# Optimization experiments

Hardware: AMD Instinct MI355X
Metric: run time of the kernel (lower is better)

The kernel has to match this reference:

```python
import jax, jax.numpy as jnp
import numpy as np

NUM_EXPERTS = 8
TOP_K = 2
RMS_EPS = 1e-6
SCALING = NUM_EXPERTS / TOP_K


def setup_inputs() -> dict:
    key = jax.random.key(0)
    ks = jax.random.split(key, 6)
    B, S, H, I, E = 4, 2048, 2048, 1024, NUM_EXPERTS
    return {
        "hidden_states": jax.random.normal(ks[0], (B, S, H), dtype=jnp.float32),
        "norm_w": jnp.ones((H,), dtype=jnp.float32),
        "router_w": jax.random.normal(ks[1], (E, H), dtype=jnp.float32) * 0.02,
        "gate_w": jax.random.normal(ks[2], (E, I, H), dtype=jnp.float32) * 0.02,
        "up_w": jax.random.normal(ks[3], (E, I, H), dtype=jnp.float32) * 0.02,
        "down_w": jax.random.normal(ks[4], (E, H, I), dtype=jnp.float32) * 0.02,
    }


def reference(hidden_states, norm_w, router_w, gate_w, up_w, down_w):
    B, S, H = hidden_states.shape
    T = B * S
    flat = hidden_states.reshape(T, H)

    # RMSNorm on router input (fp32 math, as in torch module)
    x32 = flat.astype(jnp.float32)
    var = jnp.mean(x32 * x32, axis=-1, keepdims=True)
    router_input = norm_w * (x32 * jax.lax.rsqrt(var + RMS_EPS))

    # Router: softmax -> top-k -> renormalize
    logits = router_input @ router_w.T                     # [T, E]
    probs = jax.nn.softmax(logits, axis=-1)
    topw, topi = jax.lax.top_k(probs, TOP_K)               # [T, K]
    topw = topw / jnp.sum(topw, axis=-1, keepdims=True)

    # Expert combine: per-token weight for expert e (0 if not selected).
    # Running every token through every expert with weight-0 masking is
    # mathematically identical to the gather/scatter dispatch.
    out = jnp.zeros_like(flat)
    for e in range(NUM_EXPERTS):
        w_e = jnp.sum(jnp.where(topi == e, topw, 0.0), axis=-1)   # [T]
        g = flat @ gate_w[e].T                                    # [T, I]
        u = flat @ up_w[e].T                                      # [T, I]
        o = (jax.nn.silu(g) * u) @ down_w[e].T                    # [T, H]
        out = out + o * w_e[:, None]

    student_output = out.reshape(B, S, H) * SCALING

    # Aux load-balancing loss (training path)
    importance = jnp.sum(probs, axis=0) / T                       # [E]
    load = jnp.sum(topi[..., None] == jnp.arange(NUM_EXPERTS), axis=(0, 1)) / (T * TOP_K)
    aux_loss = jnp.sum(importance * load.astype(jnp.float32)) * NUM_EXPERTS

    return student_output, aux_loss
```

## Files before the change

### kernel.cpp

```cpp
#include <hip/hip_runtime.h>
#include <hip/hip_bf16.h>
#include <cstdint>

#define T_TOKENS 8192
#define H_DIM 2048
#define I_DIM 1024
#define N_EXPERTS 8
#define PAIRS (T_TOKENS * 2)
#define TOT_TILES 144
#define TOT_ROWS (TOT_TILES * 128)

using f32x4 = __attribute__((ext_vector_type(4))) float;
using bfv   = __attribute__((ext_vector_type(8))) short;
using u16x8 = __attribute__((ext_vector_type(8))) unsigned short;
using u32x4 = __attribute__((ext_vector_type(4))) unsigned int;

typedef __attribute__((address_space(3))) unsigned int lds_u32;
typedef __attribute__((address_space(1))) unsigned int glb_u32;

__device__ __forceinline__ void gll16(const void* g, void* l) {
  __builtin_amdgcn_global_load_lds((const glb_u32*)g, (lds_u32*)l, 16, 0, 0);
}
#define SB0() __builtin_amdgcn_sched_barrier(0)
#define BAR() __builtin_amdgcn_s_barrier()

__device__ inline unsigned short f2bf(float f) {
  unsigned int u = __float_as_uint(f);
  u += 0x7FFFu + ((u >> 16) & 1u);
  return (unsigned short)(u >> 16);
}
__device__ __forceinline__ unsigned int pkbf(float lo, float hi) {
  unsigned int r;
  asm("v_cvt_pk_bf16_f32 %0, %1, %2" : "=v"(r) : "v"(lo), "v"(hi));
  return r;
}

__global__ __launch_bounds__(256) void moe_convert_kernel(
    const float* __restrict__ src, unsigned short* __restrict__ dst, int n8) {
  int i = blockIdx.x * 256 + threadIdx.x;
  if (i >= n8) return;
  size_t o = (size_t)i * 8;
  f32x4 a = *reinterpret_cast<const f32x4*>(src + o);
  f32x4 b = *reinterpret_cast<const f32x4*>(src + o + 4);
  u16x8 r = {f2bf(a[0]), f2bf(a[1]), f2bf(a[2]), f2bf(a[3]),
             f2bf(b[0]), f2bf(b[1]), f2bf(b[2]), f2bf(b[3])};
  *reinterpret_cast<u16x8*>(dst + o) = r;
}

__global__ __launch_bounds__(256) void moe_router_kernel(
    const float* __restrict__ X, const float* __restrict__ norm_w,
    const float* __restrict__ rw, float* __restrict__ probs,
    float* __restrict__ topw, int* __restrict__ topi,
    unsigned int* __restrict__ counts) {
  int t = blockIdx.x;
  int tid = threadIdx.x;
  const float* x = X + (size_t)t * H_DIM;
  int base = tid * 8;
  f32x4 v0 = *reinterpret_cast<const f32x4*>(x + base);
  f32x4 v1 = *reinterpret_cast<const f32x4*>(x + base + 4);
  f32x4 nw0 = *reinterpret_cast<const f32x4*>(norm_w + base);
  f32x4 nw1 = *reinterpret_cast<const f32x4*>(norm_w + base + 4);
  float vals[9];
  vals[0] = v0[0]*v0[0] + v0[1]*v0[1] + v0[2]*v0[2] + v0[3]*v0[3]
          + v1[0]*v1[0] + v1[1]*v1[1] + v1[2]*v1[2] + v1[3]*v1[3];
  f32x4 a0 = v0 * nw0, a1 = v1 * nw1;
#pragma unroll
  for (int e = 0; e < 8; ++e) {
    const float* r = rw + e * H_DIM + base;
    f32x4 r0 = *reinterpret_cast<const f32x4*>(r);
    f32x4 r1 = *reinterpret_cast<const f32x4*>(r + 4);
    f32x4 d = a0 * r0 + a1 * r1;
    vals[e + 1] = d[0] + d[1] + d[2] + d[3];
  }
#pragma unroll
  for (int v = 0; v < 9; ++v) {
    float s = vals[v];
#pragma unroll
    for (int off = 32; off > 0; off >>= 1) s += __shfl_xor(s, off);
    vals[v] = s;
  }
  __shared__ float red[4][9];
  int lane = tid & 63, w = tid >> 6;
  if (lane == 0) {
#pragma unroll
    for (int v = 0; v < 9; ++v) red[w][v] = vals[v];
  }
  __syncthreads();
  if (tid == 0) {
    float tot[9];
#pragma unroll
    for (int v = 0; v < 9; ++v) tot[v] = red[0][v] + red[1][v] + red[2][v] + red[3][v];
    float rs = rsqrtf(tot[0] / (float)H_DIM + 1e-6f);
    float lg[8], mx = -1e30f;
#pragma unroll
    for (int e = 0; e < 8; ++e) { lg[e] = tot[e + 1] * rs; mx = fmaxf(mx, lg[e]); }
    float pe[8], sum = 0.f;
#pragma unroll
    for (int e = 0; e < 8; ++e) { pe[e] = expf(lg[e] - mx); sum += pe[e]; }
    float inv = 1.f / sum;
#pragma unroll
    for (int e = 0; e < 8; ++e) { pe[e] *= inv; probs[t * 8 + e] = pe[e]; }
    int b1 = 0; float p1 = pe[0];
#pragma unroll
    for (int e = 1; e < 8; ++e) if (pe[e] > p1) { p1 = pe[e]; b1 = e; }
    int b2 = -1; float p2 = -1.f;
#pragma unroll
    for (int e = 0; e < 8; ++e) if (e != b1 && pe[e] > p2) { p2 = pe[e]; b2 = e; }
    float wsum = p1 + p2;
    topw[t * 2] = p1 / wsum;
    topw[t * 2 + 1] = p2 / wsum;
    topi[t * 2] = b1;
    topi[t * 2 + 1] = b2;
    atomicAdd(&counts[b1], 1u);
    atomicAdd(&counts[8 + b2], 1u);
  }
}

__global__ __launch_bounds__(256) void moe_importance_kernel(
    const float* __restrict__ probs, float* __restrict__ impSum) {
  int e = blockIdx.x, tid = threadIdx.x;
  float s = 0.f;
  for (int t = tid; t < T_TOKENS; t += 256) s += probs[t * 8 + e];
  __shared__ float red[256];
  red[tid] = s;
  __syncthreads();
  for (int st = 128; st > 0; st >>= 1) {
    if (tid < st) red[tid] += red[tid + st];
    __syncthreads();
  }
  if (tid == 0) impSum[e] = red[0];
}

__global__ void moe_offsets_aux_kernel(const unsigned int* __restrict__ counts,
                                       const float* __restrict__ impSum,
                                       int* __restrict__ tileOff,
                                       float* __restrict__ out_aux) {
  if (threadIdx.x == 0 && blockIdx.x == 0) {
    int acc = 0;
    for (int b = 0; b < 16; ++b) {
      tileOff[b] = acc;
      acc += (int)((counts[b] + 127u) >> 7);
    }
    tileOff[16] = acc;
    float a = 0.f;
    for (int e = 0; e < 8; ++e) {
      float load = (float)(counts[e] + counts[8 + e]) / (float)PAIRS;
      a += (impSum[e] / (float)T_TOKENS) * load;
    }
    out_aux[0] = a * (float)N_EXPERTS;
  }
}

__global__ __launch_bounds__(256) void moe_assign_kernel(
    const int* __restrict__ topi, const int* __restrict__ tileOff,
    unsigned int* __restrict__ cursors, int* __restrict__ row2pair) {
  int p = blockIdx.x * 256 + threadIdx.x;
  if (p >= PAIRS) return;
  int b = topi[p] + 8 * (p & 1);
  unsigned int pos = atomicAdd(&cursors[b], 1u);
  row2pair[tileOff[b] * 128 + (int)pos] = p;
}

__global__ __launch_bounds__(512, 2) void moe_stage_a(
    const float* __restrict__ X,
    const unsigned short* __restrict__ Wg, const unsigned short* __restrict__ Wu,
    const int* __restrict__ row2pair, const int* __restrict__ tileOff,
    unsigned int* __restrict__ workCtr, unsigned short* __restrict__ P) {
  __shared__ __align__(16) unsigned short sAB[2][24576];
  __shared__ int sTok[128];
  __shared__ int sWork;
  const int tid = threadIdx.x;
  const int lane = tid & 63, w = tid >> 6;
  const int wm = w >> 2, wn = w & 3;
  const int lrow = lane & 15, grp = lane >> 4;
  const int rloc = lane >> 3, cch = lane & 7;
  const int swz8 = (cch ^ rloc) * 8;
  const int ar = tid >> 2, aq = tid & 3;
  const int ach0 = ((aq * 2) ^ (ar & 7)) * 8;
  const int ach1 = ((aq * 2 + 1) ^ (ar & 7)) * 8;
  const int nTiles = tileOff[16];
  const int nWork = nTiles * 8;

  for (;;) {
    if (tid == 0) sWork = (int)atomicAdd(workCtr, 1u);
    __syncthreads();
    const int item = sWork;
    if (item >= nWork) break;
    const int mt = item % nTiles;
    const int nt = item / nTiles;
    int b = 0;
#pragma unroll
    for (int k = 1; k < 16; ++k) if (tileOff[k] <= mt) b = k;
    const int e = b & 7;
    const int row0 = mt * 128, n0 = nt * 128;
    if (tid < 128) {
      int pr = row2pair[row0 + tid];
      sTok[tid] = (pr >= 0) ? (pr >> 1) : 0;
    }
    __syncthreads();

    const float* aSrc = X + (size_t)sTok[ar] * H_DIM + aq * 16;
    const unsigned short* bSrc[4];
    const size_t wbase = (size_t)e * ((size_t)I_DIM * H_DIM);
#pragma unroll
    for (int i = 0; i < 4; ++i) {
      int s = 4 * w + i;
      int col = n0 + (s >> 3) * 32 + (s & 3) * 8 + rloc;
      const unsigned short* basep = (s & 4) ? Wu : Wg;
      bSrc[i] = basep + wbase + (size_t)col * H_DIM + swz8;
    }
    const int bDst = 8192 + 4 * w * 512 + lane * 8;

    f32x4 acc[4][4] = {};

    {
      f32x4 a0 = *reinterpret_cast<const f32x4*>(aSrc);
      f32x4 a1 = *reinterpret_cast<const f32x4*>(aSrc + 4);
      f32x4 a2 = *reinterpret_cast<const f32x4*>(aSrc + 8);
      f32x4 a3 = *reinterpret_cast<const f32x4*>(aSrc + 12);
      SB0();
#pragma unroll
      for (int i = 0; i < 4; ++i)
        gll16(bSrc[i], (void*)&sAB[0][bDst + i * 512]);
      SB0();
      u32x4 q0 = {pkbf(a0[0], a0[1]), pkbf(a0[2], a0[3]), pkbf(a1[0], a1[1]), pkbf(a1[2], a1[3])};
      u32x4 q1 = {pkbf(a2[0], a2[1]), pkbf(a2[2], a2[3]), pkbf(a3[0], a3[1]), pkbf(a3[2], a3[3])};
      *reinterpret_cast<u32x4*>(&sAB[0][ar * 64 + ach0]) = q0;
      *reinterpret_cast<u32x4*>(&sAB[0][ar * 64 + ach1]) = q1;
      asm volatile("s_waitcnt lgkmcnt(0)" ::: "memory");
      SB0();
      BAR();
      SB0();
    }

    int cur = 0;
#pragma unroll 1
    for (int kk = 0; kk < 32; ++kk) {
      f32x4 a0, a1, a2, a3;
      if (kk < 31) {
        const float* ap = aSrc + (kk + 1) * 64;
        a0 = *reinterpret_cast<const f32x4*>(ap);
        a1 = *reinterpret_cast<const f32x4*>(ap + 4);
        a2 = *reinterpret_cast<const f32x4*>(ap + 8);
        a3 = *reinterpret_cast<const f32x4*>(ap + 12);
        SB0();
#pragma unroll
        for (int i = 0; i < 4; ++i)
          gll16(bSrc[i] + (kk + 1) * 64, (void*)&sAB[cur ^ 1][bDst + i * 512]);
        SB0();
        asm volatile("s_waitcnt vmcnt(8)" ::: "memory");
      } else {
        asm volatile("s_waitcnt vmcnt(0)" ::: "memory");
      }
      SB0();
      BAR();
      SB0();
#pragma unroll
      for (int ks = 0; ks < 2; ++ks) {
        bfv af[4], bf[4];
        const int co = ((ks * 4 + grp) ^ cch) << 3;
#pragma unroll
        for (int m = 0; m < 4; ++m) {
          int r = wm * 64 + m * 16 + lrow;
          af[m] = *reinterpret_cast<const bfv*>(&sAB[cur][r * 64 + co]);
        }
#pragma unroll
        for (int n = 0; n < 4; ++n) {
          int R = wn * 64 + n * 16 + lrow;
          bf[n] = *reinterpret_cast<const bfv*>(&sAB[cur][8192 + R * 64 + co]);
        }
#pragma unroll
        for (int m = 0; m < 4; ++m)
#pragma unroll
          for (int n = 0; n < 4; ++n)
            acc[m][n] = __builtin_amdgcn_mfma_f32_16x16x32_bf16(af[m], bf[n], acc[m][n], 0, 0, 0);
      }
      if (kk < 31) {
        u32x4 q0 = {pkbf(a0[0], a0[1]), pkbf(a0[2], a0[3]), pkbf(a1[0], a1[1]), pkbf(a1[2], a1[3])};
        u32x4 q1 = {pkbf(a2[0], a2[1]), pkbf(a2[2], a2[3]), pkbf(a3[0], a3[1]), pkbf(a3[2], a3[3])};
        *reinterpret_cast<u32x4*>(&sAB[cur ^ 1][ar * 64 + ach0]) = q0;
        *reinterpret_cast<u32x4*>(&sAB[cur ^ 1][ar * 64 + ach1]) = q1;
        asm volatile("s_waitcnt lgkmcnt(0)" ::: "memory");
      }
      SB0();
      BAR();
      cur ^= 1;
    }

    const int rb = grp * 4;
#pragma unroll
    for (int m = 0; m < 4; ++m) {
#pragma unroll
      for (int n = 0; n < 2; ++n) {
#pragma unroll
        for (int j = 0; j < 4; ++j) {
          float g = acc[m][n][j];
          float uu = acc[m][n + 2][j];
          float pv = (g / (1.f + expf(-g))) * uu;
          int rl = wm * 64 + m * 16 + rb + j;
          int cl = n0 + wn * 32 + n * 16 + lrow;
          P[(size_t)(row0 + rl) * I_DIM + cl] = f2bf(pv);
        }
      }
    }
  }
}

__global__ __launch_bounds__(512, 2) void moe_stage_b(
    const unsigned short* __restrict__ Pb, const unsigned short* __restrict__ Wd,
    const int* __restrict__ row2pair, const int* __restrict__ tileOff,
    const float* __restrict__ topw, unsigned int* __restrict__ workCtr,
    float* __restrict__ out, int phase) {
  __shared__ __align__(16) unsigned short sAB[2][24576];
  __shared__ int sPair[128];
  __shared__ int sWork;
  const int tid = threadIdx.x;
  const int lane = tid & 63, w = tid >> 6;
  const int wm = w >> 2, wn = w & 3;
  const int lrow = lane & 15, grp = lane >> 4;
  const int rloc = lane >> 3, cch = lane & 7;
  const int swz8 = (cch ^ rloc) * 8;
  const int t0 = phase ? tileOff[8] : 0;
  const int t1 = phase ? tileOff[16] : tileOff[8];
  const int nTiles = t1 - t0;
  const int nWork = nTiles * 8;
  const int ldsOff = 6 * w * 512 + lane * 8;

  for (;;) {
    if (tid == 0) sWork = (int)atomicAdd(workCtr, 1u);
    __syncthreads();
    const int item = sWork;
    if (item >= nWork) break;
    const int mt = t0 + item % nTiles;
    const int nt = item / nTiles;
    int b = 0;
#pragma unroll
    for (int k = 1; k < 16; ++k) if (tileOff[k] <= mt) b = k;
    const int e = b & 7;
    const int row0 = mt * 128, h0 = nt * 256;
    if (tid < 128) sPair[tid] = row2pair[row0 + tid];
    __syncthreads();

    const unsigned short* src[6];
#pragma unroll
    for (int i = 0; i < 6; ++i) {
      int s = 6 * w + i;
      if (s < 16) {
        src[i] = Pb + (size_t)(row0 + s * 8 + rloc) * I_DIM + swz8;
      } else {
        int sb = s - 16;
        src[i] = Wd + (size_t)e * ((size_t)H_DIM * I_DIM) +
                 (size_t)(h0 + sb * 8 + rloc) * I_DIM + swz8;
      }
    }
    f32x4 acc[4][4] = {};

#pragma unroll
    for (int i = 0; i < 6; ++i)
      gll16(src[i], (void*)&sAB[0][ldsOff + i * 512]);

    int cur = 0;
#pragma unroll 1
    for (int kk = 0; kk < 16; ++kk) {
      if (kk < 15) {
#pragma unroll
        for (int i = 0; i < 6; ++i)
          gll16(src[i] + (kk + 1) * 64, (void*)&sAB[cur ^ 1][ldsOff + i * 512]);
        SB0();
        asm volatile("s_waitcnt vmcnt(6)" ::: "memory");
      } else {
        asm volatile("s_waitcnt vmcnt(0)" ::: "memory");
      }
      SB0();
      BAR();
      SB0();
#pragma unroll
      for (int ks = 0; ks < 2; ++ks) {
        bfv af[4], bf[4];
        const int co = ((ks * 4 + grp) ^ cch) << 3;
#pragma unroll
        for (int m = 0; m < 4; ++m) {
          int r = wm * 64 + m * 16 + lrow;
          af[m] = *reinterpret_cast<const bfv*>(&sAB[cur][r * 64 + co]);
        }
#pragma unroll
        for (int n = 0; n < 4; ++n) {
          int R = wn * 64 + n * 16 + lrow;
          bf[n] = *reinterpret_cast<const bfv*>(&sAB[cur][8192 + R * 64 + co]);
        }
#pragma unroll
        for (int m = 0; m < 4; ++m)
#pragma unroll
          for (int n = 0; n < 4; ++n)
            acc[m][n] = __builtin_amdgcn_mfma_f32_16x16x32_bf16(af[m], bf[n], acc[m][n], 0, 0, 0);
      }
      SB0();
      BAR();
      cur ^= 1;
    }

    const int rb = grp * 4;
#pragma unroll
    for (int m = 0; m < 4; ++m) {
#pragma unroll
      for (int j = 0; j < 4; ++j) {
        int rl = wm * 64 + m * 16 + rb + j;
        int pr = sPair[rl];
        if (pr < 0) continue;
        float wgt = topw[pr] * 4.f;
        float* orow = out + (size_t)(pr >> 1) * H_DIM + h0 + wn * 64 + lrow;
        if (phase) {
#pragma unroll
          for (int n = 0; n < 4; ++n) orow[n * 16] += wgt * acc[m][n][j];
        } else {
#pragma unroll
          for (int n = 0; n < 4; ++n) orow[n * 16] = wgt * acc[m][n][j];
        }
      }
    }
  }
}

extern "C" void kernel_launch(void* const* d_in, const int* in_sizes, int n_in,
                              void* d_out, int out_size, void* d_ws, size_t ws_size,
                              hipStream_t stream) {
  const float* X = (const float*)d_in[0];
  const float* norm_w = (const float*)d_in[1];
  const float* router_w = (const float*)d_in[2];
  const float* gate_w = (const float*)d_in[3];
  const float* up_w = (const float*)d_in[4];
  const float* down_w = (const float*)d_in[5];
  float* out = (float*)d_out;

  char* ws = (char*)d_ws;
  unsigned short* P = (unsigned short*)(ws);
  float* probs = (float*)(ws + 37748736);
  float* topw = (float*)(ws + 38010880);
  int* topi = (int*)(ws + 38076416);
  int* row2pair = (int*)(ws + 38141952);
  char* ctrl = ws + 38215680;
  unsigned int* counts = (unsigned int*)(ctrl);
  unsigned int* cursors = (unsigned int*)(ctrl + 64);
  float* impSum = (float*)(ctrl + 128);
  int* tileOff = (int*)(ctrl + 192);
  unsigned int* wcA = (unsigned int*)(ctrl + 384);
  unsigned int* wcB0 = (unsigned int*)(ctrl + 388);
  unsigned int* wcB1 = (unsigned int*)(ctrl + 392);
  unsigned short* W1 = (unsigned short*)(ws + 38216192);
  unsigned short* W2 = (unsigned short*)(ws + 71770624);

  hipMemsetAsync(ctrl, 0, 512, stream);
  hipMemsetAsync(row2pair, 0xFF, (size_t)TOT_ROWS * 4, stream);

  const int N8 = (N_EXPERTS * I_DIM * H_DIM) / 8;
  moe_convert_kernel<<<N8 / 256, 256, 0, stream>>>(gate_w, W1, N8);
  moe_convert_kernel<<<N8 / 256, 256, 0, stream>>>(up_w, W2, N8);

  moe_router_kernel<<<T_TOKENS, 256, 0, stream>>>(X, norm_w, router_w, probs, topw, topi, counts);
  moe_importance_kernel<<<N_EXPERTS, 256, 0, stream>>>(probs, impSum);
  moe_offsets_aux_kernel<<<1, 64, 0, stream>>>(counts, impSum, tileOff, out + 16777216);
  moe_assign_kernel<<<PAIRS / 256, 256, 0, stream>>>(topi, tileOff, cursors, row2pair);

  moe_stage_a<<<256, 512, 0, stream>>>(X, W1, W2, row2pair, tileOff, wcA, P);
  moe_convert_kernel<<<N8 / 256, 256, 0, stream>>>(down_w, W1, N8);
  moe_stage_b<<<256, 512, 0, stream>>>(P, W1, row2pair, tileOff, topw, wcB0, out, 0);
  moe_stage_b<<<256, 512, 0, stream>>>(P, W1, row2pair, tileOff, topw, wcB1, out, 1);
}
```

Measured before the change: 769.6 us.

## Pre-convert activations to bf16 in router and retile expert GEMMs to 4-wave blocks

The router kernel now also writes a bf16 copy of the hidden states, so stage A can load A tiles straight into LDS with global_load_lds instead of loading fp32, packing to bf16 and storing through registers. Both GEMM stages switch from 8-wave 512-thread blocks with K=64 steps to 4-wave 256-thread blocks with K=32 steps. Each wave now covers all 128 rows by 32 output columns (8x4 MFMA tiles). MFMA sections are wrapped in s_setprio, and the grids double to 512 blocks. This trades one extra bf16 write of X and more K iterations for less register and conversion work in the GEMM loops and higher occupancy.

```diff
diff --git a/kernel.cpp b/kernel.cpp
--- a/kernel.cpp
+++ b/kernel.cpp
@@ -13,7 +13,6 @@
 using f32x4 = __attribute__((ext_vector_type(4))) float;
 using bfv   = __attribute__((ext_vector_type(8))) short;
 using u16x8 = __attribute__((ext_vector_type(8))) unsigned short;
-using u32x4 = __attribute__((ext_vector_type(4))) unsigned int;
 
 typedef __attribute__((address_space(3))) unsigned int lds_u32;
 typedef __attribute__((address_space(1))) unsigned int glb_u32;
@@ -28,11 +27,6 @@
   unsigned int u = __float_as_uint(f);
   u += 0x7FFFu + ((u >> 16) & 1u);
   return (unsigned short)(u >> 16);
-}
-__device__ __forceinline__ unsigned int pkbf(float lo, float hi) {
-  unsigned int r;
-  asm("v_cvt_pk_bf16_f32 %0, %1, %2" : "=v"(r) : "v"(lo), "v"(hi));
-  return r;
 }
 
 __global__ __launch_bounds__(256) void moe_convert_kernel(
@@ -51,13 +45,16 @@
     const float* __restrict__ X, const float* __restrict__ norm_w,
     const float* __restrict__ rw, float* __restrict__ probs,
     float* __restrict__ topw, int* __restrict__ topi,
-    unsigned int* __restrict__ counts) {
+    unsigned int* __restrict__ counts, unsigned short* __restrict__ Xb) {
   int t = blockIdx.x;
   int tid = threadIdx.x;
   const float* x = X + (size_t)t * H_DIM;
   int base = tid * 8;
   f32x4 v0 = *reinterpret_cast<const f32x4*>(x + base);
   f32x4 v1 = *reinterpret_cast<const f32x4*>(x + base + 4);
+  u16x8 bx = {f2bf(v0[0]), f2bf(v0[1]), f2bf(v0[2]), f2bf(v0[3]),
+              f2bf(v1[0]), f2bf(v1[1]), f2bf(v1[2]), f2bf(v1[3])};
+  *reinterpret_cast<u16x8*>(Xb + (size_t)t * H_DIM + base) = bx;
   f32x4 nw0 = *reinterpret_cast<const f32x4*>(norm_w + base);
   f32x4 nw1 = *reinterpret_cast<const f32x4*>(norm_w + base + 4);
   float vals[9];
@@ -161,23 +158,20 @@
   row2pair[tileOff[b] * 128 + (int)pos] = p;
 }
 
-__global__ __launch_bounds__(512, 2) void moe_stage_a(
-    const float* __restrict__ X,
+
+__global__ __launch_bounds__(256, 2) void moe_stage_a(
+    const unsigned short* __restrict__ Xb,
     const unsigned short* __restrict__ Wg, const unsigned short* __restrict__ Wu,
     const int* __restrict__ row2pair, const int* __restrict__ tileOff,
     unsigned int* __restrict__ workCtr, unsigned short* __restrict__ P) {
-  __shared__ __align__(16) unsigned short sAB[2][24576];
+  __shared__ __align__(16) unsigned short sAB[2][12288];
   __shared__ int sTok[128];
   __shared__ int sWork;
   const int tid = threadIdx.x;
   const int lane = tid & 63, w = tid >> 6;
-  const int wm = w >> 2, wn = w & 3;
   const int lrow = lane & 15, grp = lane >> 4;
-  const int rloc = lane >> 3, cch = lane & 7;
-  const int swz8 = (cch ^ rloc) * 8;
-  const int ar = tid >> 2, aq = tid & 3;
-  const int ach0 = ((aq * 2) ^ (ar & 7)) * 8;
-  const int ach1 = ((aq * 2 + 1) ^ (ar & 7)) * 8;
+  const int s8 = ((tid & 3) ^ ((tid >> 2) & 3)) << 3;
+  const int rsw = (grp ^ (lane & 3)) << 3;
   const int nTiles = tileOff[16];
   const int nWork = nTiles * 8;
 
@@ -192,104 +186,71 @@
 #pragma unroll
     for (int k = 1; k < 16; ++k) if (tileOff[k] <= mt) b = k;
     const int e = b & 7;
-    const int row0 = mt * 128, n0 = nt * 128;
+    const int row0 = mt * 128;
     if (tid < 128) {
       int pr = row2pair[row0 + tid];
       sTok[tid] = (pr >= 0) ? (pr >> 1) : 0;
     }
     __syncthreads();
 
-    const float* aSrc = X + (size_t)sTok[ar] * H_DIM + aq * 16;
-    const unsigned short* bSrc[4];
     const size_t wbase = (size_t)e * ((size_t)I_DIM * H_DIM);
-#pragma unroll
-    for (int i = 0; i < 4; ++i) {
-      int s = 4 * w + i;
-      int col = n0 + (s >> 3) * 32 + (s & 3) * 8 + rloc;
-      const unsigned short* basep = (s & 4) ? Wu : Wg;
-      bSrc[i] = basep + wbase + (size_t)col * H_DIM + swz8;
-    }
-    const int bDst = 8192 + 4 * w * 512 + lane * 8;
-
-    f32x4 acc[4][4] = {};
-
-    {
-      f32x4 a0 = *reinterpret_cast<const f32x4*>(aSrc);
-      f32x4 a1 = *reinterpret_cast<const f32x4*>(aSrc + 4);
-      f32x4 a2 = *reinterpret_cast<const f32x4*>(aSrc + 8);
-      f32x4 a3 = *reinterpret_cast<const f32x4*>(aSrc + 12);
-      SB0();
-#pragma unroll
-      for (int i = 0; i < 4; ++i)
-        gll16(bSrc[i], (void*)&sAB[0][bDst + i * 512]);
-      SB0();
-      u32x4 q0 = {pkbf(a0[0], a0[1]), pkbf(a0[2], a0[3]), pkbf(a1[0], a1[1]), pkbf(a1[2], a1[3])};
-      u32x4 q1 = {pkbf(a2[0], a2[1]), pkbf(a2[2], a2[3]), pkbf(a3[0], a3[1]), pkbf(a3[2], a3[3])};
-      *reinterpret_cast<u32x4*>(&sAB[0][ar * 64 + ach0]) = q0;
-      *reinterpret_cast<u32x4*>(&sAB[0][ar * 64 + ach1]) = q1;
-      asm volatile("s_waitcnt lgkmcnt(0)" ::: "memory");
-      SB0();
-      BAR();
-      SB0();
-    }
+    const unsigned short* src[6];
+#pragma unroll
+    for (int it = 0; it < 2; ++it) {
+      int ra = it * 64 + (tid >> 2);
+      src[it] = Xb + (size_t)sTok[ra] * H_DIM + s8;
+    }
+#pragma unroll
+    for (int it = 2; it < 6; ++it) {
+      int c = (it - 2) * 64 + (tid >> 2);
+      int wq = c >> 6, r6 = c & 63;
+      int irow = nt * 128 + wq * 32 + (r6 & 31);
+      const unsigned short* basep = (r6 >> 5) ? Wu : Wg;
+      src[it] = basep + wbase + (size_t)irow * H_DIM + s8;
+    }
+
+    f32x4 acc[8][4] = {};
+
+#pragma unroll
+    for (int i = 0; i < 6; ++i)
+      gll16(src[i], (void*)&sAB[0][(i * 256 + tid) * 8]);
 
     int cur = 0;
 #pragma unroll 1
-    for (int kk = 0; kk < 32; ++kk) {
-      f32x4 a0, a1, a2, a3;
-      if (kk < 31) {
-        const float* ap = aSrc + (kk + 1) * 64;
-        a0 = *reinterpret_cast<const f32x4*>(ap);
-        a1 = *reinterpret_cast<const f32x4*>(ap + 4);
-        a2 = *reinterpret_cast<const f32x4*>(ap + 8);
-        a3 = *reinterpret_cast<const f32x4*>(ap + 12);
+    for (int kk = 0; kk < 64; ++kk) {
+      if (kk < 63) {
+#pragma unroll
+        for (int i = 0; i < 6; ++i)
+          gll16(src[i] + ((kk + 1) << 5), (void*)&sAB[cur ^ 1][(i * 256 + tid) * 8]);
         SB0();
-#pragma unroll
-        for (int i = 0; i < 4; ++i)
-          gll16(bSrc[i] + (kk + 1) * 64, (void*)&sAB[cur ^ 1][bDst + i * 512]);
-        SB0();
-        asm volatile("s_waitcnt vmcnt(8)" ::: "memory");
+        asm volatile("s_waitcnt vmcnt(6)" ::: "memory");
       } else {
         asm volatile("s_waitcnt vmcnt(0)" ::: "memory");
       }
       SB0();
       BAR();
       SB0();
-#pragma unroll
-      for (int ks = 0; ks < 2; ++ks) {
-        bfv af[4], bf[4];
-        const int co = ((ks * 4 + grp) ^ cch) << 3;
-#pragma unroll
-        for (int m = 0; m < 4; ++m) {
-          int r = wm * 64 + m * 16 + lrow;
-          af[m] = *reinterpret_cast<const bfv*>(&sAB[cur][r * 64 + co]);
-        }
-#pragma unroll
-        for (int n = 0; n < 4; ++n) {
-          int R = wn * 64 + n * 16 + lrow;
-          bf[n] = *reinterpret_cast<const bfv*>(&sAB[cur][8192 + R * 64 + co]);
-        }
-#pragma unroll
-        for (int m = 0; m < 4; ++m)
-#pragma unroll
-          for (int n = 0; n < 4; ++n)
-            acc[m][n] = __builtin_amdgcn_mfma_f32_16x16x32_bf16(af[m], bf[n], acc[m][n], 0, 0, 0);
-      }
-      if (kk < 31) {
-        u32x4 q0 = {pkbf(a0[0], a0[1]), pkbf(a0[2], a0[3]), pkbf(a1[0], a1[1]), pkbf(a1[2], a1[3])};
-        u32x4 q1 = {pkbf(a2[0], a2[1]), pkbf(a2[2], a2[3]), pkbf(a3[0], a3[1]), pkbf(a3[2], a3[3])};
-        *reinterpret_cast<u32x4*>(&sAB[cur ^ 1][ar * 64 + ach0]) = q0;
-        *reinterpret_cast<u32x4*>(&sAB[cur ^ 1][ar * 64 + ach1]) = q1;
-        asm volatile("s_waitcnt lgkmcnt(0)" ::: "memory");
-      }
+      bfv af[8], bf[4];
+#pragma unroll
+      for (int m = 0; m < 8; ++m)
+        af[m] = *reinterpret_cast<const bfv*>(&sAB[cur][(m * 16 + lrow) * 32 + rsw]);
+#pragma unroll
+      for (int n = 0; n < 4; ++n)
+        bf[n] = *reinterpret_cast<const bfv*>(&sAB[cur][4096 + (w * 64 + n * 16 + lrow) * 32 + rsw]);
+      __builtin_amdgcn_s_setprio(1);
+#pragma unroll
+      for (int m = 0; m < 8; ++m)
+#pragma unroll
+        for (int n = 0; n < 4; ++n)
+          acc[m][n] = __builtin_amdgcn_mfma_f32_16x16x32_bf16(af[m], bf[n], acc[m][n], 0, 0, 0);
+      __builtin_amdgcn_s_setprio(0);
       SB0();
       BAR();
       cur ^= 1;
     }
 
-    const int rb = grp * 4;
-#pragma unroll
-    for (int m = 0; m < 4; ++m) {
+#pragma unroll
+    for (int m = 0; m < 8; ++m) {
 #pragma unroll
       for (int n = 0; n < 2; ++n) {
 #pragma unroll
@@ -297,34 +258,32 @@
           float g = acc[m][n][j];
           float uu = acc[m][n + 2][j];
           float pv = (g / (1.f + expf(-g))) * uu;
-          int rl = wm * 64 + m * 16 + rb + j;
-          int cl = n0 + wn * 32 + n * 16 + lrow;
-          P[(size_t)(row0 + rl) * I_DIM + cl] = f2bf(pv);
+          int row = row0 + m * 16 + grp * 4 + j;
+          int col = nt * 128 + w * 32 + n * 16 + lrow;
+          P[(size_t)row * I_DIM + col] = f2bf(pv);
         }
       }
     }
   }
 }
 
-__global__ __launch_bounds__(512, 2) void moe_stage_b(
+__global__ __launch_bounds__(256, 2) void moe_stage_b(
     const unsigned short* __restrict__ Pb, const unsigned short* __restrict__ Wd,
     const int* __restrict__ row2pair, const int* __restrict__ tileOff,
     const float* __restrict__ topw, unsigned int* __restrict__ workCtr,
     float* __restrict__ out, int phase) {
-  __shared__ __align__(16) unsigned short sAB[2][24576];
+  __shared__ __align__(16) unsigned short sAB[2][12288];
   __shared__ int sPair[128];
   __shared__ int sWork;
   const int tid = threadIdx.x;
   const int lane = tid & 63, w = tid >> 6;
-  const int wm = w >> 2, wn = w & 3;
   const int lrow = lane & 15, grp = lane >> 4;
-  const int rloc = lane >> 3, cch = lane & 7;
-  const int swz8 = (cch ^ rloc) * 8;
+  const int s8 = ((tid & 3) ^ ((tid >> 2) & 3)) << 3;
+  const int rsw = (grp ^ (lane & 3)) << 3;
   const int t0 = phase ? tileOff[8] : 0;
   const int t1 = phase ? tileOff[16] : tileOff[8];
   const int nTiles = t1 - t0;
   const int nWork = nTiles * 8;
-  const int ldsOff = 6 * w * 512 + lane * 8;
 
   for (;;) {
     if (tid == 0) sWork = (int)atomicAdd(workCtr, 1u);
@@ -343,29 +302,29 @@
 
     const unsigned short* src[6];
 #pragma unroll
-    for (int i = 0; i < 6; ++i) {
-      int s = 6 * w + i;
-      if (s < 16) {
-        src[i] = Pb + (size_t)(row0 + s * 8 + rloc) * I_DIM + swz8;
-      } else {
-        int sb = s - 16;
-        src[i] = Wd + (size_t)e * ((size_t)H_DIM * I_DIM) +
-                 (size_t)(h0 + sb * 8 + rloc) * I_DIM + swz8;
-      }
-    }
-    f32x4 acc[4][4] = {};
+    for (int it = 0; it < 2; ++it) {
+      int ra = it * 64 + (tid >> 2);
+      src[it] = Pb + (size_t)(row0 + ra) * I_DIM + s8;
+    }
+#pragma unroll
+    for (int it = 2; it < 6; ++it) {
+      int c = (it - 2) * 64 + (tid >> 2);
+      src[it] = Wd + (size_t)e * ((size_t)H_DIM * I_DIM) + (size_t)(h0 + c) * I_DIM + s8;
+    }
+
+    f32x4 acc[8][4] = {};
 
 #pragma unroll
     for (int i = 0; i < 6; ++i)
-      gll16(src[i], (void*)&sAB[0][ldsOff + i * 512]);
+      gll16(src[i], (void*)&sAB[0][(i * 256 + tid) * 8]);
 
     int cur = 0;
 #pragma unroll 1
-    for (int kk = 0; kk < 16; ++kk) {
-      if (kk < 15) {
+    for (int kk = 0; kk < 32; ++kk) {
+      if (kk < 31) {
 #pragma unroll
         for (int i = 0; i < 6; ++i)
-          gll16(src[i] + (kk + 1) * 64, (void*)&sAB[cur ^ 1][ldsOff + i * 512]);
+          gll16(src[i] + ((kk + 1) << 5), (void*)&sAB[cur ^ 1][(i * 256 + tid) * 8]);
         SB0();
         asm volatile("s_waitcnt vmcnt(6)" ::: "memory");
       } else {
@@ -374,41 +333,34 @@
       SB0();
       BAR();
       SB0();
-#pragma unroll
-      for (int ks = 0; ks < 2; ++ks) {
-        bfv af[4], bf[4];
-        const int co = ((ks * 4 + grp) ^ cch) << 3;
-#pragma unroll
-        for (int m = 0; m < 4; ++m) {
-          int r = wm * 64 + m * 16 + lrow;
-          af[m] = *reinterpret_cast<const bfv*>(&sAB[cur][r * 64 + co]);
-        }
-#pragma unroll
-        for (int n = 0; n < 4; ++n) {
-          int R = wn * 64 + n * 16 + lrow;
-          bf[n] = *reinterpret_cast<const bfv*>(&sAB[cur][8192 + R * 64 + co]);
-        }
-#pragma unroll
-        for (int m = 0; m < 4; ++m)
-#pragma unroll
-          for (int n = 0; n < 4; ++n)
-            acc[m][n] = __builtin_amdgcn_mfma_f32_16x16x32_bf16(af[m], bf[n], acc[m][n], 0, 0, 0);
-      }
+      bfv af[8], bf[4];
+#pragma unroll
+      for (int m = 0; m < 8; ++m)
+        af[m] = *reinterpret_cast<const bfv*>(&sAB[cur][(m * 16 + lrow) * 32 + rsw]);
+#pragma unroll
+      for (int n = 0; n < 4; ++n)
+        bf[n] = *reinterpret_cast<const bfv*>(&sAB[cur][4096 + (w * 64 + n * 16 + lrow) * 32 + rsw]);
+      __builtin_amdgcn_s_setprio(1);
+#pragma unroll
+      for (int m = 0; m < 8; ++m)
+#pragma unroll
+        for (int n = 0; n < 4; ++n)
+          acc[m][n] = __builtin_amdgcn_mfma_f32_16x16x32_bf16(af[m], bf[n], acc[m][n], 0, 0, 0);
+      __builtin_amdgcn_s_setprio(0);
       SB0();
       BAR();
       cur ^= 1;
     }
 
-    const int rb = grp * 4;
-#pragma unroll
-    for (int m = 0; m < 4; ++m) {
+#pragma unroll
+    for (int m = 0; m < 8; ++m) {
 #pragma unroll
       for (int j = 0; j < 4; ++j) {
-        int rl = wm * 64 + m * 16 + rb + j;
+        int rl = m * 16 + grp * 4 + j;
         int pr = sPair[rl];
         if (pr < 0) continue;
         float wgt = topw[pr] * 4.f;
-        float* orow = out + (size_t)(pr >> 1) * H_DIM + h0 + wn * 64 + lrow;
+        float* orow = out + (size_t)(pr >> 1) * H_DIM + h0 + w * 64 + lrow;
         if (phase) {
 #pragma unroll
           for (int n = 0; n < 4; ++n) orow[n * 16] += wgt * acc[m][n][j];
@@ -448,6 +400,7 @@
   unsigned int* wcB1 = (unsigned int*)(ctrl + 392);
   unsigned short* W1 = (unsigned short*)(ws + 38216192);
   unsigned short* W2 = (unsigned short*)(ws + 71770624);
+  unsigned short* Xb = (unsigned short*)(ws + 105325056);
 
   hipMemsetAsync(ctrl, 0, 512, stream);
   hipMemsetAsync(row2pair, 0xFF, (size_t)TOT_ROWS * 4, stream);
@@ -456,13 +409,14 @@
   moe_convert_kernel<<<N8 / 256, 256, 0, stream>>>(gate_w, W1, N8);
   moe_convert_kernel<<<N8 / 256, 256, 0, stream>>>(up_w, W2, N8);
 
-  moe_router_kernel<<<T_TOKENS, 256, 0, stream>>>(X, norm_w, router_w, probs, topw, topi, counts);
+  moe_router_kernel<<<T_TOKENS, 256, 0, stream>>>(X, norm_w, router_w, probs, topw, topi,
+                                                  counts, Xb);
   moe_importance_kernel<<<N_EXPERTS, 256, 0, stream>>>(probs, impSum);
   moe_offsets_aux_kernel<<<1, 64, 0, stream>>>(counts, impSum, tileOff, out + 16777216);
   moe_assign_kernel<<<PAIRS / 256, 256, 0, stream>>>(topi, tileOff, cursors, row2pair);
 
-  moe_stage_a<<<256, 512, 0, stream>>>(X, W1, W2, row2pair, tileOff, wcA, P);
+  moe_stage_a<<<512, 256, 0, stream>>>(Xb, W1, W2, row2pair, tileOff, wcA, P);
   moe_convert_kernel<<<N8 / 256, 256, 0, stream>>>(down_w, W1, N8);
-  moe_stage_b<<<256, 512, 0, stream>>>(P, W1, row2pair, tileOff, topw, wcB0, out, 0);
-  moe_stage_b<<<256, 512, 0, stream>>>(P, W1, row2pair, tileOff, topw, wcB1, out, 1);
-}
+  moe_stage_b<<<512, 256, 0, stream>>>(P, W1, row2pair, tileOff, topw, wcB0, out, 0);
+  moe_stage_b<<<512, 256, 0, stream>>>(P, W1, row2pair, tileOff, topw, wcB1, out, 1);
+}
```

After: 707.1 us (median of 2 runs). -8.1%, faster.
